# Kernel optimization log

Hardware: AMD Instinct MI355X
Metric: run time of the kernel (lower is better)

The kernel has to match this reference:

```python
import jax, jax.numpy as jnp
import numpy as np

DIM = 256
NUM_HEADS = 4
HEAD_DIM = DIM // NUM_HEADS
SCALE = HEAD_DIM ** -0.5
LN_EPS = 1e-5


def setup_inputs() -> dict:
    key = jax.random.key(0)
    ks = jax.random.split(key, 12)
    V, B, C, H, W = 3, 2, DIM, 32, 32
    s = 0.02
    return {
        "features": jax.random.normal(ks[0], (V, B, C, H, W), jnp.float32),
        "Wq": jax.random.normal(ks[1], (DIM, DIM), jnp.float32) * s,
        "bq": jnp.zeros((DIM,), jnp.float32),
        "Wk": jax.random.normal(ks[2], (DIM, DIM), jnp.float32) * s,
        "bk": jnp.zeros((DIM,), jnp.float32),
        "Wv": jax.random.normal(ks[3], (DIM, DIM), jnp.float32) * s,
        "bv": jnp.zeros((DIM,), jnp.float32),
        "Wp": jax.random.normal(ks[4], (DIM, DIM), jnp.float32) * s,
        "bp": jnp.zeros((DIM,), jnp.float32),
        "gamma": jnp.ones((DIM,), jnp.float32),
        "beta": jnp.zeros((DIM,), jnp.float32),
    }


def reference(features, Wq, bq, Wk, bk, Wv, bv, Wp, bp, gamma, beta):
    V, B, C, H, W = features.shape
    N = H * W
    L = V * N
    # concat views along token axis: [B, V*N, C]
    x = features.reshape(V, B, C, N).transpose(1, 0, 3, 2).reshape(B, L, C)
    # QKV projections (torch Linear: x @ W.T + b)
    q = (x @ Wq.T + bq).reshape(B, L, NUM_HEADS, HEAD_DIM).transpose(0, 2, 1, 3)
    k = (x @ Wk.T + bk).reshape(B, L, NUM_HEADS, HEAD_DIM).transpose(0, 2, 1, 3)
    v = (x @ Wv.T + bv).reshape(B, L, NUM_HEADS, HEAD_DIM).transpose(0, 2, 1, 3)
    # full attention (chunked loop in original is exact, dropout off in eval)
    attn = jax.nn.softmax(jnp.einsum('bhqd,bhkd->bhqk', q, k) * SCALE, axis=-1)
    o = jnp.einsum('bhqk,bhkd->bhqd', attn, v)  # [B, H, L, D]
    o = o.transpose(0, 2, 1, 3).reshape(B, L, C)
    # output proj + LayerNorm
    o = o @ Wp.T + bp
    mu = jnp.mean(o, axis=-1, keepdims=True)
    var = jnp.mean(jnp.square(o - mu), axis=-1, keepdims=True)
    o = (o - mu) * jax.lax.rsqrt(var + LN_EPS) * gamma + beta
    # mean over views, back to [B, C, H, W]
    o = o.reshape(B, V, N, C).mean(axis=1)
    return o.reshape(B, H, W, C).transpose(0, 3, 1, 2)
```

## Files before the change

### kernel.cpp

```cpp
#include <hip/hip_runtime.h>
#include <hip/hip_bf16.h>

#define V_ 3
#define B_ 2
#define C_ 256
#define N_ 1024
#define L_ 3072
#define NH 4
#define DH 64
#define SCALE 0.125f
#define LOG2E 1.44269504088896340736f

typedef __attribute__((ext_vector_type(8))) short short8;
typedef __attribute__((ext_vector_type(4))) float floatx4;
typedef unsigned short u16;
typedef unsigned int u32;

__device__ __forceinline__ u16 f2bf(float f) {
    union { float f; u32 u; } c; c.f = f;
    u32 u = c.u;
    u32 lsb = (u >> 16) & 1u;
    u += 0x7fffu + lsb;
    return (u16)(u >> 16);
}
__device__ __forceinline__ u32 pk_bf16(float a, float b) {
    __hip_bfloat162 h = __float22bfloat162_rn(make_float2(a, b));
    union { __hip_bfloat162 h; u32 u; } cv; cv.h = h; return cv.u;
}

__global__ __launch_bounds__(256) void k_prep_gather(
    const float* __restrict__ feat,
    const float* __restrict__ Wq, const float* __restrict__ Wk,
    const float* __restrict__ Wv, const float* __restrict__ Wp,
    u16* __restrict__ x, u16* __restrict__ Wb) {
    int bid = blockIdx.x;
    int t = threadIdx.x;
    if (bid < 384) {
        __shared__ u16 tile[64][66];
        int n0 = (bid & 15) << 6;
        int c0 = ((bid >> 4) & 3) << 6;
        int b  = (bid >> 6) & 1;
        int v  = bid >> 7;
        const float* src = feat + ((size_t)((v * B_ + b) * C_ + c0)) * N_ + n0;
        for (int i = 0; i < 8; ++i) {
            int idx = i * 256 + t;
            int cl = idx >> 5;
            int np2 = idx & 31;
            float2 f = *(const float2*)(src + (size_t)cl * N_ + np2 * 2);
            *(u32*)&tile[cl][np2 * 2] = pk_bf16(f.x, f.y);
        }
        __syncthreads();
        u16* dst = x + ((size_t)(b * L_ + v * N_ + n0)) * C_ + c0;
        for (int i = 0; i < 8; ++i) {
            int idx = i * 256 + t;
            int nl = idx >> 5;
            int cl = (idx & 31) * 2;
            u32 uu = (u32)tile[cl][nl] | ((u32)tile[cl + 1][nl] << 16);
            *(u32*)(dst + (size_t)nl * C_ + cl) = uu;
        }
    } else {
        int idx = (bid - 384) * 256 + t;
        int g0 = idx * 16;
        int m = g0 >> 16;
        const float* src = (m == 0) ? Wq : (m == 1) ? Wk : (m == 2) ? Wv : Wp;
        int off = g0 & 65535;
#pragma unroll
        for (int e = 0; e < 8; ++e) {
            float2 f = *(const float2*)(src + off + e * 2);
            ((u32*)(Wb + g0))[e] = pk_bf16(f.x, f.y);
        }
    }
}

__global__ __launch_bounds__(64) void k_qkv(
    const u16* __restrict__ x, const u16* __restrict__ Wb,
    const float* __restrict__ bq, const float* __restrict__ bk,
    const float* __restrict__ bv,
    u16* __restrict__ Qf, u16* __restrict__ Kf, u16* __restrict__ Vf) {
    int bid = blockIdx.x;
    int npc = bid & 3;
    int rest = bid >> 2;
    int m  = rest / 192;
    int rb = rest % 192;
    int b  = rb / 96;
    int r0 = (rb % 96) * 32;
    int lane = threadIdx.x;
    int quad = lane >> 4, m16 = lane & 15;

    const u16* xrow0 = x + ((size_t)(b * L_ + r0 + m16)) * C_ + quad * 8;
    const u16* xrow1 = xrow0 + (size_t)16 * C_;
    short8 a0[8], a1[8];
#pragma unroll
    for (int kc = 0; kc < 8; ++kc) {
        a0[kc] = *(const short8*)(xrow0 + kc * 32);
        a1[kc] = *(const short8*)(xrow1 + kc * 32);
    }
    const u16* W = Wb + (size_t)m * 65536;

    if (m == 2) {
#pragma unroll
        for (int np = npc * 2; np < npc * 2 + 2; ++np) {
            int nt0 = np * 2;
            const u16* w0 = W + (size_t)(nt0 * 16 + m16) * C_ + quad * 8;
            const u16* w1 = w0 + 16 * C_;
            short8 wf0[8], wf1[8];
#pragma unroll
            for (int kc = 0; kc < 8; ++kc) {
                wf0[kc] = *(const short8*)(w0 + kc * 32);
                wf1[kc] = *(const short8*)(w1 + kc * 32);
            }
            floatx4 acc00 = {0.f,0.f,0.f,0.f}, acc01 = {0.f,0.f,0.f,0.f};
            floatx4 acc10 = {0.f,0.f,0.f,0.f}, acc11 = {0.f,0.f,0.f,0.f};
#pragma unroll
            for (int kc = 0; kc < 8; ++kc) {
                acc00 = __builtin_amdgcn_mfma_f32_16x16x32_bf16(a0[kc], wf0[kc], acc00, 0, 0, 0);
                acc01 = __builtin_amdgcn_mfma_f32_16x16x32_bf16(a0[kc], wf1[kc], acc01, 0, 0, 0);
                acc10 = __builtin_amdgcn_mfma_f32_16x16x32_bf16(a1[kc], wf0[kc], acc10, 0, 0, 0);
                acc11 = __builtin_amdgcn_mfma_f32_16x16x32_bf16(a1[kc], wf1[kc], acc11, 0, 0, 0);
            }
#pragma unroll
            for (int gi = 0; gi < 2; ++gi)
#pragma unroll
            for (int half = 0; half < 2; ++half) {
                int dout = (nt0 + half) * 16 + m16;
                float bias = bv[dout];
                int h = dout >> 6, dh = dout & 63;
                size_t bh = (size_t)(b * NH + h);
                floatx4 acc = gi ? (half ? acc11 : acc10) : (half ? acc01 : acc00);
                float f0 = acc[0] + bias, f1 = acc[1] + bias;
                float f2 = acc[2] + bias, f3 = acc[3] + bias;
                int lr0 = r0 + gi * 16 + quad * 4;
                int tile = lr0 >> 6, kk = lr0 & 63;
                int halfv = kk >> 5, quadp = (kk >> 3) & 3, j0 = kk & 7;
                int ntv = dh >> 4, m16pp = dh & 15;
                u32* p = (u32*)(Vf + (bh * 48 + tile) * 4096 +
                                ((size_t)((ntv * 2 + halfv) * 64 + quadp * 16 + m16pp)) * 8 + j0);
                p[0] = pk_bf16(f0, f1);
                p[1] = pk_bf16(f2, f3);
            }
        }
    } else {
        const float* bs = (m == 0) ? bq : bk;
        float scale = (m == 0) ? (SCALE * LOG2E) : 1.0f;
#pragma unroll
        for (int np = npc * 2; np < npc * 2 + 2; ++np) {
            int nt0 = np * 2;
            const u16* w0 = W + (size_t)(nt0 * 16 + m16) * C_ + quad * 8;
            const u16* w1 = w0 + 16 * C_;
            short8 wf0[8], wf1[8];
#pragma unroll
            for (int kc = 0; kc < 8; ++kc) {
                wf0[kc] = *(const short8*)(w0 + kc * 32);
                wf1[kc] = *(const short8*)(w1 + kc * 32);
            }
            floatx4 acc00 = {0.f,0.f,0.f,0.f}, acc01 = {0.f,0.f,0.f,0.f};
            floatx4 acc10 = {0.f,0.f,0.f,0.f}, acc11 = {0.f,0.f,0.f,0.f};
#pragma unroll
            for (int kc = 0; kc < 8; ++kc) {
                acc00 = __builtin_amdgcn_mfma_f32_16x16x32_bf16(wf0[kc], a0[kc], acc00, 0, 0, 0);
                acc01 = __builtin_amdgcn_mfma_f32_16x16x32_bf16(wf0[kc], a1[kc], acc01, 0, 0, 0);
                acc10 = __builtin_amdgcn_mfma_f32_16x16x32_bf16(wf1[kc], a0[kc], acc10, 0, 0, 0);
                acc11 = __builtin_amdgcn_mfma_f32_16x16x32_bf16(wf1[kc], a1[kc], acc11, 0, 0, 0);
            }
#pragma unroll
            for (int tt = 0; tt < 2; ++tt)
#pragma unroll
            for (int gi = 0; gi < 2; ++gi) {
                int ntb = (nt0 + tt) * 16;
                int h = ntb >> 6;
                size_t bh = (size_t)(b * NH + h);
                int dh0 = (ntb & 63) + quad * 4;
                int cc = dh0 >> 5, qp = (dh0 >> 3) & 3, j0 = dh0 & 7;
                float4 b4 = *(const float4*)(bs + ntb + quad * 4);
                floatx4 acc = tt ? (gi ? acc11 : acc10) : (gi ? acc01 : acc00);
                float f0 = (acc[0] + b4.x) * scale, f1 = (acc[1] + b4.y) * scale;
                float f2 = (acc[2] + b4.z) * scale, f3 = (acc[3] + b4.w) * scale;
                uint2 pk;
                pk.x = pk_bf16(f0, f1);
                pk.y = pk_bf16(f2, f3);
                int token = r0 + gi * 16 + m16;
                if (m == 0) {
                    int grp = (r0 >> 4) + gi;
                    *(uint2*)(Qf + (bh * 192 + grp) * 1024 +
                              (size_t)(cc * 64 + qp * 16 + m16) * 8 + j0) = pk;
                } else {
                    int tile = token >> 6;
                    int ntk = ((r0 & 63) >> 4) + gi;
                    *(uint2*)(Kf + (bh * 48 + tile) * 4096 +
                              (size_t)((ntk * 2 + cc) * 64 + qp * 16 + m16) * 8 + j0) = pk;
                }
            }
        }
    }
}

__global__ __launch_bounds__(256, 3) void k_attn(
    const u16* __restrict__ Qf, const u16* __restrict__ Kf,
    const u16* __restrict__ Vf, float* __restrict__ o_p, float* __restrict__ l_p) {
    __shared__ __align__(16) char smem[36864];
    __shared__ float l_red[3][3][16];
    u16* PL = (u16*)smem;
    float* o_red = (float*)smem;
    int bid = blockIdx.x;
    int rest = bid & 511;
    int s  = bid >> 9;
    int qt = rest & 63;
    int h  = (rest >> 6) & 3;
    int b  = rest >> 8;
    int lane = threadIdx.x & 63;
    int w    = threadIdx.x >> 6;
    int quad = lane >> 4, m16 = lane & 15;
    size_t bh = (size_t)(b * NH + h);

    const u16* qbase = Qf + (bh * 192 + qt * 3) * 1024 + (size_t)lane * 8;
    const u16* kbase = Kf + bh * 48 * 4096 + (size_t)lane * 8;
    const u16* vbase = Vf + bh * 48 * 4096 + (size_t)lane * 8;

    short8 aq[3][2];
#pragma unroll
    for (int g = 0; g < 3; ++g) {
        aq[g][0] = *(const short8*)(qbase + g * 1024);
        aq[g][1] = *(const short8*)(qbase + g * 1024 + 512);
    }

    float l_s[3] = {0.f, 0.f, 0.f};
    floatx4 o_acc[3][4];
#pragma unroll
    for (int g = 0; g < 3; ++g)
#pragma unroll
        for (int nt = 0; nt < 4; ++nt) o_acc[g][nt] = (floatx4){0.f, 0.f, 0.f, 0.f};

    int kt0 = s * 24 + w * 6;
    short8 kv[8];

    for (int i = 0; i < 6; ++i) {
        size_t tbase = (size_t)(kt0 + i) * 4096;
#pragma unroll
        for (int f = 0; f < 8; ++f)
            kv[f] = *(const short8*)(kbase + tbase + f * 512);
#pragma unroll
        for (int g = 0; g < 3; ++g) {
            floatx4 sx[4];
#pragma unroll
            for (int nt = 0; nt < 4; ++nt) {
                floatx4 z = {0.f, 0.f, 0.f, 0.f};
                z = __builtin_amdgcn_mfma_f32_16x16x32_bf16(kv[nt * 2], aq[g][0], z, 0, 0, 0);
                sx[nt] = __builtin_amdgcn_mfma_f32_16x16x32_bf16(kv[nt * 2 + 1], aq[g][1], z, 0, 0, 0);
            }
            u16* plrow = PL + (((w * 3 + g) * 16) + m16) * 72;
            float lsum = 0.f;
#pragma unroll
            for (int nt = 0; nt < 4; ++nt) {
                float p0 = __builtin_amdgcn_exp2f(sx[nt][0]);
                float p1 = __builtin_amdgcn_exp2f(sx[nt][1]);
                float p2 = __builtin_amdgcn_exp2f(sx[nt][2]);
                float p3 = __builtin_amdgcn_exp2f(sx[nt][3]);
                lsum += (p0 + p1) + (p2 + p3);
                uint2 pk; pk.x = pk_bf16(p0, p1); pk.y = pk_bf16(p2, p3);
                *(uint2*)(plrow + nt * 16 + quad * 4) = pk;
            }
            l_s[g] += lsum;
        }
#pragma unroll
        for (int f = 0; f < 8; ++f)
            kv[f] = *(const short8*)(vbase + tbase + f * 512);
#pragma unroll
        for (int g = 0; g < 3; ++g) {
            const u16* plrow = PL + (((w * 3 + g) * 16) + m16) * 72;
            short8 bp0 = *(const short8*)(plrow + quad * 8);
            short8 bp1 = *(const short8*)(plrow + 32 + quad * 8);
#pragma unroll
            for (int nt = 0; nt < 4; ++nt) {
                o_acc[g][nt] = __builtin_amdgcn_mfma_f32_16x16x32_bf16(kv[nt * 2], bp0, o_acc[g][nt], 0, 0, 0);
                o_acc[g][nt] = __builtin_amdgcn_mfma_f32_16x16x32_bf16(kv[nt * 2 + 1], bp1, o_acc[g][nt], 0, 0, 0);
            }
        }
    }
    float l_row[3];
#pragma unroll
    for (int g = 0; g < 3; ++g) {
        float ps = l_s[g];
        ps += __shfl_xor(ps, 16);
        ps += __shfl_xor(ps, 32);
        l_row[g] = ps;
    }
    __syncthreads();
    if (w > 0) {
#pragma unroll
        for (int g = 0; g < 3; ++g) {
#pragma unroll
            for (int nt = 0; nt < 4; ++nt)
                *(floatx4*)&o_red[(((w - 1) * 3 + g) * 4 + nt) * 256 + lane * 4] = o_acc[g][nt];
            if (quad == 0) l_red[w - 1][g][m16] = l_row[g];
        }
    }
    __syncthreads();
    if (w == 0) {
#pragma unroll
        for (int g = 0; g < 3; ++g) {
            if (quad == 0)
                l_p[(size_t)bid * 48 + g * 16 + m16] =
                    l_row[g] + l_red[0][g][m16] + l_red[1][g][m16] + l_red[2][g][m16];
#pragma unroll
            for (int nt = 0; nt < 4; ++nt) {
                floatx4 tot = o_acc[g][nt];
#pragma unroll
                for (int w1 = 0; w1 < 3; ++w1)
                    tot += *(const floatx4*)&o_red[((w1 * 3 + g) * 4 + nt) * 256 + lane * 4];
                *(floatx4*)&o_p[(((size_t)bid * 3 + g) * 4 + nt) * 256 + lane * 4] = tot;
            }
        }
    }
}

__global__ __launch_bounds__(192) void k_comb(
    const float* __restrict__ o_p, const float* __restrict__ l_p,
    u16* __restrict__ o) {
    int bid = blockIdx.x;
    int qt = bid & 63;
    int h  = (bid >> 6) & 3;
    int b  = bid >> 8;
    int lane = threadIdx.x & 63;
    int g    = threadIdx.x >> 6;
    int quad = lane >> 4, m16 = lane & 15;
    float l = l_p[(size_t)bid * 48 + g * 16 + m16] +
              l_p[(size_t)(bid + 512) * 48 + g * 16 + m16];
    float lt = __builtin_amdgcn_rcpf(l);
#pragma unroll
    for (int nt = 0; nt < 4; ++nt) {
        floatx4 t0 = *(const floatx4*)&o_p[(((size_t)bid * 3 + g) * 4 + nt) * 256 + lane * 4];
        floatx4 t1 = *(const floatx4*)&o_p[(((size_t)(bid + 512) * 3 + g) * 4 + nt) * 256 + lane * 4];
        floatx4 tot = t0 + t1;
        uint2 pk;
        pk.x = pk_bf16(tot[0] * lt, tot[1] * lt);
        pk.y = pk_bf16(tot[2] * lt, tot[3] * lt);
        *(uint2*)(o + ((size_t)(b * L_ + qt * 48 + g * 16 + m16)) * C_ +
                  h * 64 + nt * 16 + quad * 4) = pk;
    }
}

__global__ __launch_bounds__(256) void k_proj_ln(
    const u16* __restrict__ o, const u16* __restrict__ Wpb,
    const float* __restrict__ bp,
    const float* __restrict__ gamma, const float* __restrict__ beta,
    u16* __restrict__ oln) {
    __shared__ float sred[4][16];
    __shared__ float sred2[4][16];
    int bid = blockIdx.x;
    int n0 = (bid & 63) << 4;
    int b  = (bid >> 6) & 1;
    int v  = bid >> 7;
    int lane = threadIdx.x & 63;
    int w    = threadIdx.x >> 6;
    int quad = lane >> 4, m16 = lane & 15;

    const u16* orow = o + ((size_t)(b * L_ + v * N_ + n0 + m16)) * C_ + quad * 8;
    short8 a[8];
#pragma unroll
    for (int kc = 0; kc < 8; ++kc) a[kc] = *(const short8*)(orow + kc * 32);

    float pr[4][4];
#pragma unroll
    for (int j = 0; j < 4; ++j) {
        int nt = w * 4 + j;
        const u16* wrow = Wpb + (size_t)(nt * 16 + m16) * C_ + quad * 8;
        floatx4 acc = {0.f, 0.f, 0.f, 0.f};
#pragma unroll
        for (int kc = 0; kc < 8; ++kc) {
            short8 bfr = *(const short8*)(wrow + kc * 32);
            acc = __builtin_amdgcn_mfma_f32_16x16x32_bf16(bfr, a[kc], acc, 0, 0, 0);
        }
        float4 b4 = *(const float4*)(bp + nt * 16 + quad * 4);
        pr[j][0] = acc[0] + b4.x; pr[j][1] = acc[1] + b4.y;
        pr[j][2] = acc[2] + b4.z; pr[j][3] = acc[3] + b4.w;
    }
    float sm = 0.f;
#pragma unroll
    for (int j = 0; j < 4; ++j)
        sm += (pr[j][0] + pr[j][1]) + (pr[j][2] + pr[j][3]);
    sm += __shfl_xor(sm, 16);
    sm += __shfl_xor(sm, 32);
    if (quad == 0) sred[w][m16] = sm;
    __syncthreads();
    float mu = (sred[0][m16] + sred[1][m16] + sred[2][m16] + sred[3][m16]) * (1.0f / C_);
    float sq = 0.f;
#pragma unroll
    for (int j = 0; j < 4; ++j)
#pragma unroll
        for (int r = 0; r < 4; ++r) { float d = pr[j][r] - mu; sq += d * d; }
    sq += __shfl_xor(sq, 16);
    sq += __shfl_xor(sq, 32);
    if (quad == 0) sred2[w][m16] = sq;
    __syncthreads();
    float var = (sred2[0][m16] + sred2[1][m16] + sred2[2][m16] + sred2[3][m16]) * (1.0f / C_);
    float rs = __builtin_amdgcn_rsqf(var + 1e-5f);
#pragma unroll
    for (int j = 0; j < 4; ++j) {
        int c0 = (w * 4 + j) * 16 + quad * 4;
        float4 g4 = *(const float4*)(gamma + c0);
        float4 be4 = *(const float4*)(beta + c0);
        float f0 = (pr[j][0] - mu) * rs * g4.x + be4.x;
        float f1 = (pr[j][1] - mu) * rs * g4.y + be4.y;
        float f2 = (pr[j][2] - mu) * rs * g4.z + be4.z;
        float f3 = (pr[j][3] - mu) * rs * g4.w + be4.w;
        uint2 pk;
        pk.x = pk_bf16(f0, f1);
        pk.y = pk_bf16(f2, f3);
        *(uint2*)(oln + ((size_t)((v * B_ + b) * N_ + n0 + m16)) * C_ + c0) = pk;
    }
}

__global__ __launch_bounds__(256) void k_mean_t(
    const u16* __restrict__ oln, float* __restrict__ out) {
    __shared__ float tile[64][65];
    int bid = blockIdx.x;
    int n0 = (bid & 15) << 6;
    int c0 = ((bid >> 4) & 3) << 6;
    int b  = bid >> 6;
    int t = threadIdx.x;
    union { u32 u; float f; } cv;
    for (int i = 0; i < 16; ++i) {
        int idx = i * 256 + t;
        int nl = idx >> 6, cl = idx & 63;
        float sm = 0.f;
#pragma unroll
        for (int v = 0; v < 3; ++v) {
            u16 raw = oln[((size_t)((v * B_ + b) * N_ + n0 + nl)) * C_ + c0 + cl];
            cv.u = ((u32)raw) << 16;
            sm += cv.f;
        }
        tile[cl][nl] = sm * (1.0f / 3.0f);
    }
    __syncthreads();
    for (int i = 0; i < 16; ++i) {
        int idx = i * 256 + t;
        int cl = idx >> 6, nl = idx & 63;
        out[((size_t)(b * C_ + c0 + cl)) * N_ + n0 + nl] = tile[cl][nl];
    }
}

extern "C" void kernel_launch(void* const* d_in, const int* in_sizes, int n_in,
                              void* d_out, int out_size, void* d_ws, size_t ws_size,
                              hipStream_t stream) {
    (void)in_sizes; (void)n_in; (void)out_size; (void)ws_size;
    const float* feat  = (const float*)d_in[0];
    const float* Wq    = (const float*)d_in[1];
    const float* bq    = (const float*)d_in[2];
    const float* Wk    = (const float*)d_in[3];
    const float* bk    = (const float*)d_in[4];
    const float* Wv    = (const float*)d_in[5];
    const float* bv    = (const float*)d_in[6];
    const float* Wp    = (const float*)d_in[7];
    const float* bp    = (const float*)d_in[8];
    const float* gamma = (const float*)d_in[9];
    const float* beta  = (const float*)d_in[10];
    float* out = (float*)d_out;

    size_t SZ = (size_t)B_ * L_ * C_;
    u16* x   = (u16*)d_ws;
    u16* Qf  = x + SZ;
    u16* Kf  = Qf + SZ;
    u16* Vf  = Kf + SZ;
    u16* o   = Vf + SZ;
    u16* Wb  = o + SZ;
    u16* oln = Wb + 4 * 65536;
    float* o_p = (float*)(oln + SZ);
    float* l_p = o_p + (size_t)1024 * 3072;

    k_prep_gather<<<dim3(448), dim3(256), 0, stream>>>(feat, Wq, Wk, Wv, Wp, x, Wb);
    k_qkv<<<dim3(2304), dim3(64), 0, stream>>>(x, Wb, bq, bk, bv, Qf, Kf, Vf);
    k_attn<<<dim3(1024), dim3(256), 0, stream>>>(Qf, Kf, Vf, o_p, l_p);
    k_comb<<<dim3(512), dim3(192), 0, stream>>>(o_p, l_p, o);
    k_proj_ln<<<dim3(384), dim3(256), 0, stream>>>(o, Wb + 3 * 65536, bp, gamma, beta, oln);
    k_mean_t<<<dim3(128), dim3(256), 0, stream>>>(oln, out);
}
```

Baseline: 140.5 us.

## Drop attention split-K, fuse combine into attention, software-pipeline QK and PV

The attention kernel no longer splits keys across two blocks, so each block covers all 48 key tiles and normalizes and writes bf16 output directly. This removes the separate combine kernel and the fp32 partial-result round trip through global memory. The inner loop is software-pipelined: K for the next tile is prefetched and its scores computed into a double-buffered LDS P tile while the current PV MFMAs run. The cost is half as many blocks (512), larger LDS, and a launch bound of 2 blocks per CU, which reduces parallelism and occupancy.

```diff
diff --git a/kernel.cpp b/kernel.cpp
--- a/kernel.cpp
+++ b/kernel.cpp
@@ -194,22 +194,21 @@
     }
 }
 
-__global__ __launch_bounds__(256, 3) void k_attn(
+__global__ __launch_bounds__(256, 2) void k_attn(
     const u16* __restrict__ Qf, const u16* __restrict__ Kf,
-    const u16* __restrict__ Vf, float* __restrict__ o_p, float* __restrict__ l_p) {
-    __shared__ __align__(16) char smem[36864];
+    const u16* __restrict__ Vf, u16* __restrict__ o) {
+    __shared__ __align__(16) char smem[55296];
     __shared__ float l_red[3][3][16];
     u16* PL = (u16*)smem;
     float* o_red = (float*)smem;
     int bid = blockIdx.x;
-    int rest = bid & 511;
-    int s  = bid >> 9;
-    int qt = rest & 63;
-    int h  = (rest >> 6) & 3;
-    int b  = rest >> 8;
+    int qt = bid & 63;
+    int h  = (bid >> 6) & 3;
+    int b  = bid >> 8;
     int lane = threadIdx.x & 63;
     int w    = threadIdx.x >> 6;
     int quad = lane >> 4, m16 = lane & 15;
+    int q0 = qt * 48;
     size_t bh = (size_t)(b * NH + h);
 
     const u16* qbase = Qf + (bh * 192 + qt * 3) * 1024 + (size_t)lane * 8;
@@ -230,49 +229,84 @@
 #pragma unroll
         for (int nt = 0; nt < 4; ++nt) o_acc[g][nt] = (floatx4){0.f, 0.f, 0.f, 0.f};
 
-    int kt0 = s * 24 + w * 6;
-    short8 kv[8];
-
-    for (int i = 0; i < 6; ++i) {
+    int kt0 = w * 12;
+    short8 kb[8], vb[8];
+
+#pragma unroll
+    for (int f = 0; f < 8; ++f)
+        kb[f] = *(const short8*)(kbase + (size_t)kt0 * 4096 + f * 512);
+#pragma unroll
+    for (int g = 0; g < 3; ++g) {
+        floatx4 sx[4];
+#pragma unroll
+        for (int nt = 0; nt < 4; ++nt) {
+            floatx4 z = {0.f, 0.f, 0.f, 0.f};
+            z = __builtin_amdgcn_mfma_f32_16x16x32_bf16(kb[nt * 2], aq[g][0], z, 0, 0, 0);
+            sx[nt] = __builtin_amdgcn_mfma_f32_16x16x32_bf16(kb[nt * 2 + 1], aq[g][1], z, 0, 0, 0);
+        }
+        u16* plrow = PL + ((0 * 12 + w * 3 + g) * 16 + m16) * 72;
+        float lsum = 0.f;
+#pragma unroll
+        for (int nt = 0; nt < 4; ++nt) {
+            float p0 = __builtin_amdgcn_exp2f(sx[nt][0]);
+            float p1 = __builtin_amdgcn_exp2f(sx[nt][1]);
+            float p2 = __builtin_amdgcn_exp2f(sx[nt][2]);
+            float p3 = __builtin_amdgcn_exp2f(sx[nt][3]);
+            lsum += (p0 + p1) + (p2 + p3);
+            uint2 pk; pk.x = pk_bf16(p0, p1); pk.y = pk_bf16(p2, p3);
+            *(uint2*)(plrow + nt * 16 + quad * 4) = pk;
+        }
+        l_s[g] += lsum;
+    }
+
+    for (int i = 0; i < 12; ++i) {
+        int cur = i & 1, nxt = cur ^ 1;
         size_t tbase = (size_t)(kt0 + i) * 4096;
 #pragma unroll
         for (int f = 0; f < 8; ++f)
-            kv[f] = *(const short8*)(kbase + tbase + f * 512);
+            vb[f] = *(const short8*)(vbase + tbase + f * 512);
+        short8 bp[3][2];
 #pragma unroll
         for (int g = 0; g < 3; ++g) {
-            floatx4 sx[4];
+            const u16* plrow = PL + ((cur * 12 + w * 3 + g) * 16 + m16) * 72;
+            bp[g][0] = *(const short8*)(plrow + quad * 8);
+            bp[g][1] = *(const short8*)(plrow + 32 + quad * 8);
+        }
+        if (i < 11) {
+#pragma unroll
+            for (int f = 0; f < 8; ++f)
+                kb[f] = *(const short8*)(kbase + tbase + 4096 + f * 512);
+        }
+#pragma unroll
+        for (int g = 0; g < 3; ++g)
 #pragma unroll
             for (int nt = 0; nt < 4; ++nt) {
-                floatx4 z = {0.f, 0.f, 0.f, 0.f};
-                z = __builtin_amdgcn_mfma_f32_16x16x32_bf16(kv[nt * 2], aq[g][0], z, 0, 0, 0);
-                sx[nt] = __builtin_amdgcn_mfma_f32_16x16x32_bf16(kv[nt * 2 + 1], aq[g][1], z, 0, 0, 0);
-            }
-            u16* plrow = PL + (((w * 3 + g) * 16) + m16) * 72;
-            float lsum = 0.f;
-#pragma unroll
-            for (int nt = 0; nt < 4; ++nt) {
-                float p0 = __builtin_amdgcn_exp2f(sx[nt][0]);
-                float p1 = __builtin_amdgcn_exp2f(sx[nt][1]);
-                float p2 = __builtin_amdgcn_exp2f(sx[nt][2]);
-                float p3 = __builtin_amdgcn_exp2f(sx[nt][3]);
-                lsum += (p0 + p1) + (p2 + p3);
-                uint2 pk; pk.x = pk_bf16(p0, p1); pk.y = pk_bf16(p2, p3);
-                *(uint2*)(plrow + nt * 16 + quad * 4) = pk;
-            }
-            l_s[g] += lsum;
-        }
-#pragma unroll
-        for (int f = 0; f < 8; ++f)
-            kv[f] = *(const short8*)(vbase + tbase + f * 512);
-#pragma unroll
-        for (int g = 0; g < 3; ++g) {
-            const u16* plrow = PL + (((w * 3 + g) * 16) + m16) * 72;
-            short8 bp0 = *(const short8*)(plrow + quad * 8);
-            short8 bp1 = *(const short8*)(plrow + 32 + quad * 8);
-#pragma unroll
-            for (int nt = 0; nt < 4; ++nt) {
-                o_acc[g][nt] = __builtin_amdgcn_mfma_f32_16x16x32_bf16(kv[nt * 2], bp0, o_acc[g][nt], 0, 0, 0);
-                o_acc[g][nt] = __builtin_amdgcn_mfma_f32_16x16x32_bf16(kv[nt * 2 + 1], bp1, o_acc[g][nt], 0, 0, 0);
+                o_acc[g][nt] = __builtin_amdgcn_mfma_f32_16x16x32_bf16(vb[nt * 2], bp[g][0], o_acc[g][nt], 0, 0, 0);
+                o_acc[g][nt] = __builtin_amdgcn_mfma_f32_16x16x32_bf16(vb[nt * 2 + 1], bp[g][1], o_acc[g][nt], 0, 0, 0);
+            }
+        if (i < 11) {
+#pragma unroll
+            for (int g = 0; g < 3; ++g) {
+                floatx4 sx[4];
+#pragma unroll
+                for (int nt = 0; nt < 4; ++nt) {
+                    floatx4 z = {0.f, 0.f, 0.f, 0.f};
+                    z = __builtin_amdgcn_mfma_f32_16x16x32_bf16(kb[nt * 2], aq[g][0], z, 0, 0, 0);
+                    sx[nt] = __builtin_amdgcn_mfma_f32_16x16x32_bf16(kb[nt * 2 + 1], aq[g][1], z, 0, 0, 0);
+                }
+                u16* plrow = PL + ((nxt * 12 + w * 3 + g) * 16 + m16) * 72;
+                float lsum = 0.f;
+#pragma unroll
+                for (int nt = 0; nt < 4; ++nt) {
+                    float p0 = __builtin_amdgcn_exp2f(sx[nt][0]);
+                    float p1 = __builtin_amdgcn_exp2f(sx[nt][1]);
+                    float p2 = __builtin_amdgcn_exp2f(sx[nt][2]);
+                    float p3 = __builtin_amdgcn_exp2f(sx[nt][3]);
+                    lsum += (p0 + p1) + (p2 + p3);
+                    uint2 pk; pk.x = pk_bf16(p0, p1); pk.y = pk_bf16(p2, p3);
+                    *(uint2*)(plrow + nt * 16 + quad * 4) = pk;
+                }
+                l_s[g] += lsum;
             }
         }
     }
@@ -298,44 +332,21 @@
     if (w == 0) {
 #pragma unroll
         for (int g = 0; g < 3; ++g) {
-            if (quad == 0)
-                l_p[(size_t)bid * 48 + g * 16 + m16] =
-                    l_row[g] + l_red[0][g][m16] + l_red[1][g][m16] + l_red[2][g][m16];
+            float lt = __builtin_amdgcn_rcpf(
+                l_row[g] + l_red[0][g][m16] + l_red[1][g][m16] + l_red[2][g][m16]);
 #pragma unroll
             for (int nt = 0; nt < 4; ++nt) {
                 floatx4 tot = o_acc[g][nt];
 #pragma unroll
                 for (int w1 = 0; w1 < 3; ++w1)
                     tot += *(const floatx4*)&o_red[((w1 * 3 + g) * 4 + nt) * 256 + lane * 4];
-                *(floatx4*)&o_p[(((size_t)bid * 3 + g) * 4 + nt) * 256 + lane * 4] = tot;
-            }
-        }
-    }
-}
-
-__global__ __launch_bounds__(192) void k_comb(
-    const float* __restrict__ o_p, const float* __restrict__ l_p,
-    u16* __restrict__ o) {
-    int bid = blockIdx.x;
-    int qt = bid & 63;
-    int h  = (bid >> 6) & 3;
-    int b  = bid >> 8;
-    int lane = threadIdx.x & 63;
-    int g    = threadIdx.x >> 6;
-    int quad = lane >> 4, m16 = lane & 15;
-    float l = l_p[(size_t)bid * 48 + g * 16 + m16] +
-              l_p[(size_t)(bid + 512) * 48 + g * 16 + m16];
-    float lt = __builtin_amdgcn_rcpf(l);
-#pragma unroll
-    for (int nt = 0; nt < 4; ++nt) {
-        floatx4 t0 = *(const floatx4*)&o_p[(((size_t)bid * 3 + g) * 4 + nt) * 256 + lane * 4];
-        floatx4 t1 = *(const floatx4*)&o_p[(((size_t)(bid + 512) * 3 + g) * 4 + nt) * 256 + lane * 4];
-        floatx4 tot = t0 + t1;
-        uint2 pk;
-        pk.x = pk_bf16(tot[0] * lt, tot[1] * lt);
-        pk.y = pk_bf16(tot[2] * lt, tot[3] * lt);
-        *(uint2*)(o + ((size_t)(b * L_ + qt * 48 + g * 16 + m16)) * C_ +
-                  h * 64 + nt * 16 + quad * 4) = pk;
+                uint2 pk;
+                pk.x = pk_bf16(tot[0] * lt, tot[1] * lt);
+                pk.y = pk_bf16(tot[2] * lt, tot[3] * lt);
+                *(uint2*)(o + ((size_t)(b * L_ + q0 + g * 16 + m16)) * C_ +
+                          h * 64 + nt * 16 + quad * 4) = pk;
+            }
+        }
     }
 }
 
@@ -464,13 +475,10 @@
     u16* o   = Vf + SZ;
     u16* Wb  = o + SZ;
     u16* oln = Wb + 4 * 65536;
-    float* o_p = (float*)(oln + SZ);
-    float* l_p = o_p + (size_t)1024 * 3072;
 
     k_prep_gather<<<dim3(448), dim3(256), 0, stream>>>(feat, Wq, Wk, Wv, Wp, x, Wb);
     k_qkv<<<dim3(2304), dim3(64), 0, stream>>>(x, Wb, bq, bk, bv, Qf, Kf, Vf);
-    k_attn<<<dim3(1024), dim3(256), 0, stream>>>(Qf, Kf, Vf, o_p, l_p);
-    k_comb<<<dim3(512), dim3(192), 0, stream>>>(o_p, l_p, o);
+    k_attn<<<dim3(512), dim3(256), 0, stream>>>(Qf, Kf, Vf, o);
     k_proj_ln<<<dim3(384), dim3(256), 0, stream>>>(o, Wb + 3 * 65536, bp, gamma, beta, oln);
     k_mean_t<<<dim3(128), dim3(256), 0, stream>>>(oln, out);
 }
```

After: 137.3 us. 1.02x faster.
